# Performance work log

Measured on AMD Instinct MI355X. Metric: run time of the kernel, lower is better.

Reference implementation:

```python
import jax, jax.numpy as jnp
import numpy as np

B, N, M, E, C_IN, C_OUT = 4, 10000, 10000, 160000, 128, 128


def setup_inputs() -> dict:
    key = jax.random.key(0)
    k1, k2, k3, k4 = jax.random.split(key, 4)
    x = jax.random.normal(k1, (B, N, C_IN), dtype=jnp.float32)
    node_idx = jax.random.randint(k2, (B, 1, E), 0, N)
    hyedge_idx = jax.random.randint(k3, (B, 1, E), 0, M)
    H = jnp.concatenate([node_idx, hyedge_idx], axis=1).astype(jnp.int64)  # [B, 2, E]
    theta = jax.random.normal(k4, (C_IN, C_OUT), dtype=jnp.float32) * (1.0 / np.sqrt(C_IN))
    bias = jnp.zeros((C_OUT,), dtype=jnp.float32)
    return {"x": x, "H": H, "theta": theta, "bias": bias}


def _hyconv_single(xg, Hg):
    # xg: [N, D] (already x @ theta); Hg: [2, E]
    node_idx, hyedge_idx = Hg[0], Hg[1]
    ones = jnp.ones((E,), dtype=xg.dtype)
    # node -> hyperedge: mean over nodes incident to each hyperedge
    deg_e = jax.ops.segment_sum(ones, hyedge_idx, num_segments=M)  # [M]
    e_norm = (1.0 / deg_e)[hyedge_idx]  # [E]
    x_edge = jax.ops.segment_sum(xg[node_idx] * e_norm[:, None], hyedge_idx, num_segments=M)  # [M, D]
    # hyperedge -> node: mean over hyperedges incident to each node
    deg_n = jax.ops.segment_sum(ones, node_idx, num_segments=N)  # [N]
    n_norm = (1.0 / deg_n)[node_idx]  # [E]
    x_node = jax.ops.segment_sum(x_edge[hyedge_idx] * n_norm[:, None], node_idx, num_segments=N)  # [N, D]
    return x_node


def reference(x, H, theta, bias):
    xt = jnp.einsum('bnc,cd->bnd', x, theta)  # dense projection
    out = jax.vmap(_hyconv_single)(xt, H)  # [B, N, D]
    return out + bias
```

## Files before the change

### kernel.cpp

```cpp
#include <hip/hip_runtime.h>
#include <hip/hip_bf16.h>


#define BB 4
#define NN 10000
#define MM 10000
#define EE 160000
#define CC 128
#define BM (BB * MM)
#define BN (BB * NN)
#define NCOPY 8
#define CAPX 16

typedef unsigned short u16;
using bf16 = __hip_bfloat16;
using bf162 = __hip_bfloat162;

__global__ __launch_bounds__(256) void build_gemm_k(const int* __restrict__ H,
                                                    int* __restrict__ ctr,
                                                    u16* __restrict__ srcA,
                                                    u16* __restrict__ srcB,
                                                    const float* __restrict__ x,
                                                    const float* __restrict__ theta,
                                                    bf16* __restrict__ xt) {
    __shared__ float sTh[64 * 128];
    __shared__ float sX[32 * 128];
    const int bi = blockIdx.x;

    if (bi % 3 != 0) {
        const int j = bi - bi / 3 - 1;
        const int g = j * 256 + threadIdx.x;
        if (g >= BB * EE) return;
        const int cp = bi & 7;
        const int b = g / EE, e = g - b * EE;
        const int nd = H[b * 2 * EE + e];
        const int he = H[b * 2 * EE + EE + e];
        const int bktA = b * MM + he;
        const int s = atomicAdd(&ctr[cp * (BM + BN) + bktA], 1);
        if (s < CAPX) srcA[((size_t)cp * BM + bktA) * CAPX + s] = (u16)nd;
        const int bktB = b * NN + nd;
        const int q = atomicAdd(&ctr[cp * (BM + BN) + BM + bktB], 1);
        if (q < CAPX) srcB[((size_t)cp * BN + bktB) * CAPX + q] = (u16)he;
        return;
    }

    const int tid = threadIdx.x;
    const int row0 = (bi / 3) * 32;
    {
        const float4* src = (const float4*)&x[row0 * 128];
        float4* dst = (float4*)sX;
#pragma unroll
        for (int i = 0; i < 4; ++i) dst[tid + 256 * i] = src[tid + 256 * i];
    }
    const int cg2 = (tid & 63) * 2;
    const int rg = tid >> 6;
    float ax[8], ay[8];
#pragma unroll
    for (int r = 0; r < 8; ++r) { ax[r] = 0.f; ay[r] = 0.f; }

    for (int half = 0; half < 2; ++half) {
        __syncthreads();
        {
            const float4* src = (const float4*)&theta[half * 64 * 128];
            float4* dst = (float4*)sTh;
#pragma unroll
            for (int i = 0; i < 8; ++i) dst[tid + 256 * i] = src[tid + 256 * i];
        }
        __syncthreads();
#pragma unroll
        for (int k4 = 0; k4 < 16; ++k4) {
            const int kk = 4 * k4;
            const float2 t0 = *(const float2*)&sTh[(kk + 0) * 128 + cg2];
            const float2 t1 = *(const float2*)&sTh[(kk + 1) * 128 + cg2];
            const float2 t2 = *(const float2*)&sTh[(kk + 2) * 128 + cg2];
            const float2 t3 = *(const float2*)&sTh[(kk + 3) * 128 + cg2];
#pragma unroll
            for (int r = 0; r < 8; ++r) {
                const float4 xv =
                    *(const float4*)&sX[(rg * 8 + r) * 128 + half * 64 + kk];
                ax[r] = fmaf(xv.x, t0.x, ax[r]); ay[r] = fmaf(xv.x, t0.y, ay[r]);
                ax[r] = fmaf(xv.y, t1.x, ax[r]); ay[r] = fmaf(xv.y, t1.y, ay[r]);
                ax[r] = fmaf(xv.z, t2.x, ax[r]); ay[r] = fmaf(xv.z, t2.y, ay[r]);
                ax[r] = fmaf(xv.w, t3.x, ax[r]); ay[r] = fmaf(xv.w, t3.y, ay[r]);
            }
        }
    }
#pragma unroll
    for (int r = 0; r < 8; ++r) {
        bf162 h;
        h.x = __float2bfloat16(ax[r]);
        h.y = __float2bfloat16(ay[r]);
        *(bf162*)&xt[(size_t)(row0 + rg * 8 + r) * 128 + cg2] = h;
    }
}

__device__ __forceinline__ void gacc(const bf16* __restrict__ base, int idx, int lane,
                                     float& sx, float& sy) {
    const unsigned raw = *(const unsigned*)(base + (size_t)idx * CC + lane * 2);
    sx += __uint_as_float(raw << 16);
    sy += __uint_as_float(raw & 0xffff0000u);
}

__device__ __forceinline__ int merge_lists(const int* __restrict__ ctr,
                                           const u16* __restrict__ src,
                                           int side_off, int Bx, int wid, int lane,
                                           u16* __restrict__ buf) {
    int cnt = 0;
    if (lane < NCOPY) {
        cnt = ctr[lane * (BM + BN) + side_off + wid];
        cnt = cnt > CAPX ? CAPX : cnt;
    }
    int pre = cnt;
#pragma unroll
    for (int d = 1; d < 8; d <<= 1) {
        int o = __shfl_up(pre, d, 64);
        if (lane >= d) pre += o;
    }
    const int base = pre - cnt;
    int total = __shfl(pre, 7, 64);
    total = total > 64 ? 64 : total;
    if (lane < NCOPY && cnt) {
        const u16* lst = src + ((size_t)lane * Bx + wid) * CAPX;
        for (int j = 0; j < cnt; ++j) {
            const int p = base + j;
            if (p < 64) buf[p] = lst[j];
        }
    }
    __syncthreads();
    return total;
}

__global__ __launch_bounds__(256) void phase1_pull(const bf16* __restrict__ xt,
                                                   const int* __restrict__ ctr,
                                                   const u16* __restrict__ srcA,
                                                   bf16* __restrict__ x_edge) {
    __shared__ __align__(16) u16 buf[4 * 64];
    const int wid = (blockIdx.x * 256 + threadIdx.x) >> 6;
    const int lane = threadIdx.x & 63;
    u16* wbuf = &buf[(threadIdx.x >> 6) * 64];
    const int total = merge_lists(ctr, srcA, 0, BM, wid, lane, wbuf);

    const bf16* base = xt + (size_t)(wid / MM) * NN * CC;
    float sx = 0.f, sy = 0.f;
    int i = 0;
    for (; i + 8 <= total; i += 8) {
        const uint4 pk = *(const uint4*)&wbuf[i];
        gacc(base, pk.x & 0xffff, lane, sx, sy);
        gacc(base, pk.x >> 16, lane, sx, sy);
        gacc(base, pk.y & 0xffff, lane, sx, sy);
        gacc(base, pk.y >> 16, lane, sx, sy);
        gacc(base, pk.z & 0xffff, lane, sx, sy);
        gacc(base, pk.z >> 16, lane, sx, sy);
        gacc(base, pk.w & 0xffff, lane, sx, sy);
        gacc(base, pk.w >> 16, lane, sx, sy);
    }
    for (; i < total; ++i) gacc(base, wbuf[i], lane, sx, sy);
    const float w = total ? 1.0f / (float)total : 0.f;
    bf162 h;
    h.x = __float2bfloat16(sx * w);
    h.y = __float2bfloat16(sy * w);
    *(bf162*)&x_edge[(size_t)wid * CC + lane * 2] = h;
}

__global__ __launch_bounds__(256) void phase2_pull(const bf16* __restrict__ x_edge,
                                                   const int* __restrict__ ctr,
                                                   const u16* __restrict__ srcB,
                                                   const float* __restrict__ bias,
                                                   float* __restrict__ out) {
    __shared__ __align__(16) u16 buf[4 * 64];
    const int wid = (blockIdx.x * 256 + threadIdx.x) >> 6;
    const int lane = threadIdx.x & 63;
    u16* wbuf = &buf[(threadIdx.x >> 6) * 64];
    const int total = merge_lists(ctr, srcB, BM, BN, wid, lane, wbuf);

    const bf16* base = x_edge + (size_t)(wid / NN) * MM * CC;
    float sx = 0.f, sy = 0.f;
    int i = 0;
    for (; i + 8 <= total; i += 8) {
        const uint4 pk = *(const uint4*)&wbuf[i];
        gacc(base, pk.x & 0xffff, lane, sx, sy);
        gacc(base, pk.x >> 16, lane, sx, sy);
        gacc(base, pk.y & 0xffff, lane, sx, sy);
        gacc(base, pk.y >> 16, lane, sx, sy);
        gacc(base, pk.z & 0xffff, lane, sx, sy);
        gacc(base, pk.z >> 16, lane, sx, sy);
        gacc(base, pk.w & 0xffff, lane, sx, sy);
        gacc(base, pk.w >> 16, lane, sx, sy);
    }
    for (; i < total; ++i) gacc(base, wbuf[i], lane, sx, sy);
    const float w = total ? 1.0f / (float)total : 0.f;
    const float2 bv = *(const float2*)&bias[lane * 2];
    float2 o;
    o.x = sx * w + bv.x;
    o.y = sy * w + bv.y;
    *(float2*)&out[(size_t)wid * CC + lane * 2] = o;
}

extern "C" void kernel_launch(void* const* d_in, const int* in_sizes, int n_in,
                              void* d_out, int out_size, void* d_ws, size_t ws_size,
                              hipStream_t stream) {
    const float* x = (const float*)d_in[0];
    const int* H = (const int*)d_in[1];
    const float* theta = (const float*)d_in[2];
    const float* bias = (const float*)d_in[3];
    float* out = (float*)d_out;

    bf16* xt = (bf16*)d_ws;
    bf16* x_edge = xt + (size_t)BB * NN * CC;
    int* ctr = (int*)(x_edge + (size_t)BB * MM * CC);
    u16* srcA = (u16*)(ctr + NCOPY * (BM + BN));
    u16* srcB = srcA + (size_t)NCOPY * BM * CAPX;

    hipMemsetAsync(ctr, 0, (size_t)NCOPY * (BM + BN) * sizeof(int), stream);

    build_gemm_k<<<3750, 256, 0, stream>>>(H, ctr, srcA, srcB, x, theta, xt);
    phase1_pull<<<BM / 4, 256, 0, stream>>>(xt, ctr, srcA, x_edge);
    phase2_pull<<<BN / 4, 256, 0, stream>>>(x_edge, ctr, srcB, bias, out);
}
```

Baseline: 198.0 us.

## Swizzle gather blocks by XCD per batch and add nontemporal loads/stores

Remaps block indices in both pull kernels so each pair of XCDs (blk&7) handles a single batch, keeping that batch's gathered source rows resident in the XCD-local L2. Adds nontemporal loads of x and nontemporal stores of xt, x_edge and the output to reduce cache pollution. Shrinks the theta shared-memory tile from 64 to 32 rows and loops four times, which lowers LDS use at the cost of extra barriers. Nontemporal stores of xt and x_edge could hurt, because the next kernel gathers from those arrays.

```diff
diff --git a/kernel.cpp b/kernel.cpp
--- a/kernel.cpp
+++ b/kernel.cpp
@@ -15,6 +15,8 @@
 typedef unsigned short u16;
 using bf16 = __hip_bfloat16;
 using bf162 = __hip_bfloat162;
+typedef float f4 __attribute__((ext_vector_type(4)));
+typedef float f2 __attribute__((ext_vector_type(2)));
 
 __global__ __launch_bounds__(256) void build_gemm_k(const int* __restrict__ H,
                                                     int* __restrict__ ctr,
@@ -23,7 +25,7 @@
                                                     const float* __restrict__ x,
                                                     const float* __restrict__ theta,
                                                     bf16* __restrict__ xt) {
-    __shared__ float sTh[64 * 128];
+    __shared__ float sTh[32 * 128];
     __shared__ float sX[32 * 128];
     const int bi = blockIdx.x;
 
@@ -47,10 +49,11 @@
     const int tid = threadIdx.x;
     const int row0 = (bi / 3) * 32;
     {
-        const float4* src = (const float4*)&x[row0 * 128];
-        float4* dst = (float4*)sX;
-#pragma unroll
-        for (int i = 0; i < 4; ++i) dst[tid + 256 * i] = src[tid + 256 * i];
+        const f4* src = (const f4*)&x[row0 * 128];
+        f4* dst = (f4*)sX;
+#pragma unroll
+        for (int i = 0; i < 4; ++i)
+            dst[tid + 256 * i] = __builtin_nontemporal_load(src + tid + 256 * i);
     }
     const int cg2 = (tid & 63) * 2;
     const int rg = tid >> 6;
@@ -58,17 +61,17 @@
 #pragma unroll
     for (int r = 0; r < 8; ++r) { ax[r] = 0.f; ay[r] = 0.f; }
 
-    for (int half = 0; half < 2; ++half) {
+    for (int q = 0; q < 4; ++q) {
         __syncthreads();
         {
-            const float4* src = (const float4*)&theta[half * 64 * 128];
-            float4* dst = (float4*)sTh;
-#pragma unroll
-            for (int i = 0; i < 8; ++i) dst[tid + 256 * i] = src[tid + 256 * i];
+            const f4* src = (const f4*)&theta[q * 32 * 128];
+            f4* dst = (f4*)sTh;
+#pragma unroll
+            for (int i = 0; i < 4; ++i) dst[tid + 256 * i] = src[tid + 256 * i];
         }
         __syncthreads();
 #pragma unroll
-        for (int k4 = 0; k4 < 16; ++k4) {
+        for (int k4 = 0; k4 < 8; ++k4) {
             const int kk = 4 * k4;
             const float2 t0 = *(const float2*)&sTh[(kk + 0) * 128 + cg2];
             const float2 t1 = *(const float2*)&sTh[(kk + 1) * 128 + cg2];
@@ -77,7 +80,7 @@
 #pragma unroll
             for (int r = 0; r < 8; ++r) {
                 const float4 xv =
-                    *(const float4*)&sX[(rg * 8 + r) * 128 + half * 64 + kk];
+                    *(const float4*)&sX[(rg * 8 + r) * 128 + q * 32 + kk];
                 ax[r] = fmaf(xv.x, t0.x, ax[r]); ay[r] = fmaf(xv.x, t0.y, ay[r]);
                 ax[r] = fmaf(xv.y, t1.x, ax[r]); ay[r] = fmaf(xv.y, t1.y, ay[r]);
                 ax[r] = fmaf(xv.z, t2.x, ax[r]); ay[r] = fmaf(xv.z, t2.y, ay[r]);
@@ -90,7 +93,9 @@
         bf162 h;
         h.x = __float2bfloat16(ax[r]);
         h.y = __float2bfloat16(ay[r]);
-        *(bf162*)&xt[(size_t)(row0 + rg * 8 + r) * 128 + cg2] = h;
+        __builtin_nontemporal_store(
+            *(unsigned*)&h,
+            (unsigned*)&xt[(size_t)(row0 + rg * 8 + r) * 128 + cg2]);
     }
 }
 
@@ -130,17 +135,26 @@
     return total;
 }
 
+__device__ __forceinline__ void swz_bucket(int blk, int tid, int& b, int& wid_local4) {
+    const int xcd = blk & 7;
+    b = xcd >> 1;
+    const int jj = ((blk >> 3) << 1) | (xcd & 1);
+    wid_local4 = jj * 4 + (tid >> 6);
+}
+
 __global__ __launch_bounds__(256) void phase1_pull(const bf16* __restrict__ xt,
                                                    const int* __restrict__ ctr,
                                                    const u16* __restrict__ srcA,
                                                    bf16* __restrict__ x_edge) {
     __shared__ __align__(16) u16 buf[4 * 64];
-    const int wid = (blockIdx.x * 256 + threadIdx.x) >> 6;
+    int b, wl;
+    swz_bucket(blockIdx.x, threadIdx.x, b, wl);
+    const int wid = b * MM + wl;
     const int lane = threadIdx.x & 63;
     u16* wbuf = &buf[(threadIdx.x >> 6) * 64];
     const int total = merge_lists(ctr, srcA, 0, BM, wid, lane, wbuf);
 
-    const bf16* base = xt + (size_t)(wid / MM) * NN * CC;
+    const bf16* base = xt + (size_t)b * NN * CC;
     float sx = 0.f, sy = 0.f;
     int i = 0;
     for (; i + 8 <= total; i += 8) {
@@ -159,7 +173,8 @@
     bf162 h;
     h.x = __float2bfloat16(sx * w);
     h.y = __float2bfloat16(sy * w);
-    *(bf162*)&x_edge[(size_t)wid * CC + lane * 2] = h;
+    __builtin_nontemporal_store(*(unsigned*)&h,
+                                (unsigned*)&x_edge[(size_t)wid * CC + lane * 2]);
 }
 
 __global__ __launch_bounds__(256) void phase2_pull(const bf16* __restrict__ x_edge,
@@ -168,12 +183,14 @@
                                                    const float* __restrict__ bias,
                                                    float* __restrict__ out) {
     __shared__ __align__(16) u16 buf[4 * 64];
-    const int wid = (blockIdx.x * 256 + threadIdx.x) >> 6;
+    int b, wl;
+    swz_bucket(blockIdx.x, threadIdx.x, b, wl);
+    const int wid = b * NN + wl;
     const int lane = threadIdx.x & 63;
     u16* wbuf = &buf[(threadIdx.x >> 6) * 64];
     const int total = merge_lists(ctr, srcB, BM, BN, wid, lane, wbuf);
 
-    const bf16* base = x_edge + (size_t)(wid / NN) * MM * CC;
+    const bf16* base = x_edge + (size_t)b * MM * CC;
     float sx = 0.f, sy = 0.f;
     int i = 0;
     for (; i + 8 <= total; i += 8) {
@@ -190,10 +207,10 @@
     for (; i < total; ++i) gacc(base, wbuf[i], lane, sx, sy);
     const float w = total ? 1.0f / (float)total : 0.f;
     const float2 bv = *(const float2*)&bias[lane * 2];
-    float2 o;
+    f2 o;
     o.x = sx * w + bv.x;
     o.y = sy * w + bv.y;
-    *(float2*)&out[(size_t)wid * CC + lane * 2] = o;
+    __builtin_nontemporal_store(o, (f2*)&out[(size_t)wid * CC + lane * 2]);
 }
 
 extern "C" void kernel_launch(void* const* d_in, const int* in_sizes, int n_in,
```

New measurement: 198.1 us. About the same (+0.1%).

## Gather rows with 16-byte loads, four rows per wave, and swizzle buckets per XCD

Applied to the files above, without the earlier changes.

Each wave now gathers four neighbor rows at once, with 16 lanes per row each loading 16 bytes, then reduces across the lane groups with shuffles. Previously every lane loaded 4 bytes of one row at a time. Block indices are remapped so each XCD handles a single batch, which aims to improve L2 locality of the gathered feature table. The list merge reads each bucket with vector loads, and outputs use nontemporal stores. The cost is extra shuffle reductions and idle lanes during the stores.

```diff
diff --git a/kernel.cpp b/kernel.cpp
--- a/kernel.cpp
+++ b/kernel.cpp
@@ -15,6 +15,8 @@
 typedef unsigned short u16;
 using bf16 = __hip_bfloat16;
 using bf162 = __hip_bfloat162;
+typedef unsigned u32x4 __attribute__((ext_vector_type(4)));
+typedef float f32x4 __attribute__((ext_vector_type(4)));
 
 __global__ __launch_bounds__(256) void build_gemm_k(const int* __restrict__ H,
                                                     int* __restrict__ ctr,
@@ -94,11 +96,20 @@
     }
 }
 
-__device__ __forceinline__ void gacc(const bf16* __restrict__ base, int idx, int lane,
-                                     float& sx, float& sy) {
-    const unsigned raw = *(const unsigned*)(base + (size_t)idx * CC + lane * 2);
-    sx += __uint_as_float(raw << 16);
-    sy += __uint_as_float(raw & 0xffff0000u);
+__device__ __forceinline__ float blo(unsigned w) { return __uint_as_float(w << 16); }
+__device__ __forceinline__ float bhi(unsigned w) { return __uint_as_float(w & 0xffff0000u); }
+__device__ __forceinline__ unsigned pk2(float a, float b) {
+    bf162 h;
+    h.x = __float2bfloat16(a);
+    h.y = __float2bfloat16(b);
+    return *(unsigned*)&h;
+}
+
+__device__ __forceinline__ void acc8(const uint4 pk, float* s) {
+    s[0] += blo(pk.x); s[1] += bhi(pk.x);
+    s[2] += blo(pk.y); s[3] += bhi(pk.y);
+    s[4] += blo(pk.z); s[5] += bhi(pk.z);
+    s[6] += blo(pk.w); s[7] += bhi(pk.w);
 }
 
 __device__ __forceinline__ int merge_lists(const int* __restrict__ ctr,
@@ -121,13 +132,25 @@
     total = total > 64 ? 64 : total;
     if (lane < NCOPY && cnt) {
         const u16* lst = src + ((size_t)lane * Bx + wid) * CAPX;
-        for (int j = 0; j < cnt; ++j) {
+        const uint4 f0 = *(const uint4*)lst;
+        const uint4 f1 = *(const uint4*)(lst + 8);
+        const unsigned wd[8] = {f0.x, f0.y, f0.z, f0.w, f1.x, f1.y, f1.z, f1.w};
+#pragma unroll
+        for (int j = 0; j < CAPX; ++j) {
+            const u16 v = (u16)((j & 1) ? (wd[j >> 1] >> 16) : (wd[j >> 1] & 0xffffu));
             const int p = base + j;
-            if (p < 64) buf[p] = lst[j];
+            if (j < cnt && p < 64) buf[p] = v;
         }
     }
     __syncthreads();
     return total;
+}
+
+__device__ __forceinline__ void swz_bucket(int blk, int tid, int& b, int& wid_local4) {
+    const int xcd = blk & 7;
+    b = xcd >> 1;
+    const int jj = ((blk >> 3) << 1) | (xcd & 1);
+    wid_local4 = jj * 4 + (tid >> 6);
 }
 
 __global__ __launch_bounds__(256) void phase1_pull(const bf16* __restrict__ xt,
@@ -135,31 +158,44 @@
                                                    const u16* __restrict__ srcA,
                                                    bf16* __restrict__ x_edge) {
     __shared__ __align__(16) u16 buf[4 * 64];
-    const int wid = (blockIdx.x * 256 + threadIdx.x) >> 6;
+    int b, wl;
+    swz_bucket(blockIdx.x, threadIdx.x, b, wl);
+    const int wid = b * MM + wl;
     const int lane = threadIdx.x & 63;
     u16* wbuf = &buf[(threadIdx.x >> 6) * 64];
     const int total = merge_lists(ctr, srcA, 0, BM, wid, lane, wbuf);
 
-    const bf16* base = xt + (size_t)(wid / MM) * NN * CC;
-    float sx = 0.f, sy = 0.f;
+    const bf16* base = xt + (size_t)b * NN * CC;
+    const int g = lane >> 4;
+    const int c16 = lane & 15;
+    float s[8];
+#pragma unroll
+    for (int k = 0; k < 8; ++k) s[k] = 0.f;
     int i = 0;
-    for (; i + 8 <= total; i += 8) {
-        const uint4 pk = *(const uint4*)&wbuf[i];
-        gacc(base, pk.x & 0xffff, lane, sx, sy);
-        gacc(base, pk.x >> 16, lane, sx, sy);
-        gacc(base, pk.y & 0xffff, lane, sx, sy);
-        gacc(base, pk.y >> 16, lane, sx, sy);
-        gacc(base, pk.z & 0xffff, lane, sx, sy);
-        gacc(base, pk.z >> 16, lane, sx, sy);
-        gacc(base, pk.w & 0xffff, lane, sx, sy);
-        gacc(base, pk.w >> 16, lane, sx, sy);
-    }
-    for (; i < total; ++i) gacc(base, wbuf[i], lane, sx, sy);
+    for (; i + 4 <= total; i += 4) {
+        const int idx = wbuf[i + g];
+        const uint4 pk = *(const uint4*)(base + (size_t)idx * CC + c16 * 8);
+        acc8(pk, s);
+    }
+    if (i < total && g < total - i) {
+        const int idx = wbuf[i + g];
+        const uint4 pk = *(const uint4*)(base + (size_t)idx * CC + c16 * 8);
+        acc8(pk, s);
+    }
+#pragma unroll
+    for (int k = 0; k < 8; ++k) {
+        s[k] += __shfl_xor(s[k], 16, 64);
+        s[k] += __shfl_xor(s[k], 32, 64);
+    }
     const float w = total ? 1.0f / (float)total : 0.f;
-    bf162 h;
-    h.x = __float2bfloat16(sx * w);
-    h.y = __float2bfloat16(sy * w);
-    *(bf162*)&x_edge[(size_t)wid * CC + lane * 2] = h;
+    if (g == 0) {
+        u32x4 o;
+        o.x = pk2(s[0] * w, s[1] * w);
+        o.y = pk2(s[2] * w, s[3] * w);
+        o.z = pk2(s[4] * w, s[5] * w);
+        o.w = pk2(s[6] * w, s[7] * w);
+        __builtin_nontemporal_store(o, (u32x4*)&x_edge[(size_t)wid * CC + c16 * 8]);
+    }
 }
 
 __global__ __launch_bounds__(256) void phase2_pull(const bf16* __restrict__ x_edge,
@@ -168,32 +204,48 @@
                                                    const float* __restrict__ bias,
                                                    float* __restrict__ out) {
     __shared__ __align__(16) u16 buf[4 * 64];
-    const int wid = (blockIdx.x * 256 + threadIdx.x) >> 6;
+    int b, wl;
+    swz_bucket(blockIdx.x, threadIdx.x, b, wl);
+    const int wid = b * NN + wl;
     const int lane = threadIdx.x & 63;
     u16* wbuf = &buf[(threadIdx.x >> 6) * 64];
     const int total = merge_lists(ctr, srcB, BM, BN, wid, lane, wbuf);
 
-    const bf16* base = x_edge + (size_t)(wid / NN) * MM * CC;
-    float sx = 0.f, sy = 0.f;
+    const bf16* base = x_edge + (size_t)b * MM * CC;
+    const int g = lane >> 4;
+    const int c16 = lane & 15;
+    float s[8];
+#pragma unroll
+    for (int k = 0; k < 8; ++k) s[k] = 0.f;
     int i = 0;
-    for (; i + 8 <= total; i += 8) {
-        const uint4 pk = *(const uint4*)&wbuf[i];
-        gacc(base, pk.x & 0xffff, lane, sx, sy);
-        gacc(base, pk.x >> 16, lane, sx, sy);
-        gacc(base, pk.y & 0xffff, lane, sx, sy);
-        gacc(base, pk.y >> 16, lane, sx, sy);
-        gacc(base, pk.z & 0xffff, lane, sx, sy);
-        gacc(base, pk.z >> 16, lane, sx, sy);
-        gacc(base, pk.w & 0xffff, lane, sx, sy);
-        gacc(base, pk.w >> 16, lane, sx, sy);
-    }
-    for (; i < total; ++i) gacc(base, wbuf[i], lane, sx, sy);
+    for (; i + 4 <= total; i += 4) {
+        const int idx = wbuf[i + g];
+        const uint4 pk = *(const uint4*)(base + (size_t)idx * CC + c16 * 8);
+        acc8(pk, s);
+    }
+    if (i < total && g < total - i) {
+        const int idx = wbuf[i + g];
+        const uint4 pk = *(const uint4*)(base + (size_t)idx * CC + c16 * 8);
+        acc8(pk, s);
+    }
+#pragma unroll
+    for (int k = 0; k < 8; ++k) {
+        s[k] += __shfl_xor(s[k], 16, 64);
+        s[k] += __shfl_xor(s[k], 32, 64);
+    }
     const float w = total ? 1.0f / (float)total : 0.f;
-    const float2 bv = *(const float2*)&bias[lane * 2];
-    float2 o;
-    o.x = sx * w + bv.x;
-    o.y = sy * w + bv.y;
-    *(float2*)&out[(size_t)wid * CC + lane * 2] = o;
+    if (g < 2) {
+        const float4 bv = *(const float4*)&bias[c16 * 8 + g * 4];
+        f32x4 o;
+        if (g == 0) {
+            o.x = s[0] * w + bv.x; o.y = s[1] * w + bv.y;
+            o.z = s[2] * w + bv.z; o.w = s[3] * w + bv.w;
+        } else {
+            o.x = s[4] * w + bv.x; o.y = s[5] * w + bv.y;
+            o.z = s[6] * w + bv.z; o.w = s[7] * w + bv.w;
+        }
+        __builtin_nontemporal_store(o, (f32x4*)&out[(size_t)wid * CC + c16 * 8 + g * 4]);
+    }
 }
 
 extern "C" void kernel_launch(void* const* d_in, const int* in_sizes, int n_in,
```

Result: faster. 184.5 us (-6.8%).
